# Performance work log

Measured on AMD Instinct MI355X. Metric: run time of the kernel, lower is better.

## Reference

```python
import jax, jax.numpy as jnp
import numpy as np

N_HEADS = 32
N_KV_HEADS = 8
HEAD_DIM = 128
HIDDEN = 4096
ROPE_BASE = 10000.0


def _rope_tables(seq_len, head_dim, base):
    inv_freq = 1.0 / (base ** (jnp.arange(0, head_dim, 2, dtype=jnp.float32) / head_dim))
    t = jnp.arange(seq_len, dtype=jnp.float32)
    freqs = jnp.outer(t, inv_freq)                    # (S, D/2)
    emb = jnp.concatenate([freqs, freqs], axis=-1)    # (S, D)
    return jnp.cos(emb), jnp.sin(emb)


def _rotate_half(x):
    half = x.shape[-1] // 2
    return jnp.concatenate([-x[..., half:], x[..., :half]], axis=-1)


def _apply_rope(x, cos, sin):
    # x: (B, H, S, D); cos/sin: (S, D)
    return x * cos[None, None] + _rotate_half(x) * sin[None, None]


def setup_inputs() -> dict:
    key = jax.random.key(0)
    k1, k2, k3 = jax.random.split(key, 3)
    bsz, q_len = 2, 2048
    total_heads = N_HEADS + 2 * N_KV_HEADS
    hidden_states = jax.random.normal(k1, (bsz, q_len, HIDDEN), dtype=jnp.float32)
    w_qkv = jax.random.normal(k2, (total_heads * HEAD_DIM, HIDDEN), dtype=jnp.float32) * 0.02
    w_o = jax.random.normal(k3, (HIDDEN, N_HEADS * HEAD_DIM), dtype=jnp.float32) * 0.02
    return {"hidden_states": hidden_states, "w_qkv": w_qkv, "w_o": w_o}


def reference(hidden_states, w_qkv, w_o):
    bsz, q_len, _ = hidden_states.shape
    n_rep = N_HEADS // N_KV_HEADS

    qkv = jnp.einsum('bsh,oh->bso', hidden_states, w_qkv)  # (B, S, total_heads*D)
    q_sz = N_HEADS * HEAD_DIM
    kv_sz = N_KV_HEADS * HEAD_DIM
    q = qkv[..., :q_sz].reshape(bsz, q_len, N_HEADS, HEAD_DIM).transpose(0, 2, 1, 3)
    k = qkv[..., q_sz:q_sz + kv_sz].reshape(bsz, q_len, N_KV_HEADS, HEAD_DIM).transpose(0, 2, 1, 3)
    v = qkv[..., q_sz + kv_sz:].reshape(bsz, q_len, N_KV_HEADS, HEAD_DIM).transpose(0, 2, 1, 3)

    cos, sin = _rope_tables(q_len, HEAD_DIM, ROPE_BASE)
    q = _apply_rope(q, cos, sin)
    k = _apply_rope(k, cos, sin)

    # repeat KV heads for GQA
    k = jnp.repeat(k, n_rep, axis=1)  # (B, H, S, D)
    v = jnp.repeat(v, n_rep, axis=1)

    scale = HEAD_DIM ** -0.5
    scores = jnp.einsum('bhqd,bhkd->bhqk', q, k) * scale
    causal = jnp.tril(jnp.ones((q_len, q_len), dtype=bool))
    scores = jnp.where(causal[None, None], scores, jnp.finfo(scores.dtype).min)
    attn = jax.nn.softmax(scores, axis=-1)
    out = jnp.einsum('bhqk,bhkd->bhqd', attn, v)  # (B, H, S, D)
    out = out.transpose(0, 2, 1, 3).reshape(bsz, q_len, N_HEADS * HEAD_DIM)
    return jnp.einsum('bso,ho->bsh', out, w_o)
```

## Files before the change

kernel.cpp:

```cpp
#include <hip/hip_runtime.h>
#include <stdint.h>

#define N_HEADS   32
#define N_KV      8
#define HEAD_DIM  128
#define HIDDEN_DIM 4096
#define BSZ       2
#define SEQ       2048
#define TOT_HEADS 48
#define QKV_DIM   6144
#define ROWS      4096
#define ROPE_HEADS 40

typedef __attribute__((ext_vector_type(4)))  float f32x4;
typedef __attribute__((ext_vector_type(16))) float f32x16;
typedef __attribute__((ext_vector_type(8)))  short bf16x8;
typedef unsigned short u16;
typedef unsigned int   u32;

#define AS1 __attribute__((address_space(1)))
#define AS3 __attribute__((address_space(3)))

static __device__ __forceinline__ float bf16f(u16 u) { return __uint_as_float(((u32)u) << 16); }
static __device__ __forceinline__ u16 f2bf(float f) {
  u32 x = __float_as_uint(f);
  x += 0x7fffu + ((x >> 16) & 1u);
  return (u16)(x >> 16);
}
static __device__ __forceinline__ u32 cvt_pk_bf16(float lo, float hi) {
  u32 r;
  asm("v_cvt_pk_bf16_f32 %0, %1, %2" : "=v"(r) : "v"(lo), "v"(hi));
  return r;
}
static __device__ __forceinline__ bf16x8 mk8(u32 a, u32 b, u32 c, u32 d) {
  union { u32 u[4]; bf16x8 v; } x;
  x.u[0] = a; x.u[1] = b; x.u[2] = c; x.u[3] = d;
  return x.v;
}
static __device__ __forceinline__ void pl32swap(u32& a, u32& b) {
  asm("v_permlane32_swap_b32 %0, %1" : "+v"(a), "+v"(b));
}
static __device__ __forceinline__ float crosshalf_max(float v) {
  u32 xa = __float_as_uint(v), xb;
  asm("v_mov_b32 %0, %1" : "=v"(xb) : "v"(xa));
  pl32swap(xa, xb);
  return fmaxf(__uint_as_float(xa), __uint_as_float(xb));
}
static __device__ __forceinline__ float crosshalf_sum(float v) {
  u32 xa = __float_as_uint(v), xb;
  asm("v_mov_b32 %0, %1" : "=v"(xb) : "v"(xa));
  pl32swap(xa, xb);
  return __uint_as_float(xa) + __uint_as_float(xb);
}

#define SB0()   __builtin_amdgcn_sched_barrier(0)
#define SBAR()  do { __builtin_amdgcn_sched_barrier(0); __builtin_amdgcn_s_barrier(); \
                     __builtin_amdgcn_sched_barrier(0); } while (0)
#define LGKM(n) do { asm volatile("s_waitcnt lgkmcnt(" #n ")" ::: "memory"); \
                     __builtin_amdgcn_sched_barrier(0); } while (0)

__global__ void cast3_k(const float4* __restrict__ a, const float4* __restrict__ b,
                        const float4* __restrict__ c,
                        ushort4* __restrict__ oa, ushort4* __restrict__ ob,
                        ushort4* __restrict__ oc, int na, int nb, int nc) {
  int i = blockIdx.x * blockDim.x + threadIdx.x;
  const int stride = gridDim.x * blockDim.x;
  const int tot = na + nb + nc;
  for (; i < tot; i += stride) {
    const float4* s; ushort4* d; int j = i;
    if (j < na)           { s = a; d = oa; }
    else if (j < na + nb) { s = b; d = ob; j -= na; }
    else                  { s = c; d = oc; j -= na + nb; }
    const float4 v = s[j];
    ushort4 o;
    o.x = f2bf(v.x); o.y = f2bf(v.y); o.z = f2bf(v.z); o.w = f2bf(v.w);
    d[j] = o;
  }
}

__global__ void rope_tables_k(float* __restrict__ ctab, float* __restrict__ stab) {
  int t = blockIdx.x * blockDim.x + threadIdx.x;
  if (t >= SEQ * 64) return;
  int s = t >> 6, i = t & 63;
  float inv = powf(10000.0f, -(float)i / 64.0f);
  float ang = (float)s * inv;
  float sv, cv;
  sincosf(ang, &sv, &cv);
  ctab[t] = cv; stab[t] = sv;
}

template<int F32OUT>
__global__ __launch_bounds__(256, 2)
void gemm_bt_k(const u16* __restrict__ A, const u16* __restrict__ Bw,
               void* __restrict__ C, int M, int N, int K, int ldc)
{
  __shared__ uint4 smA[1024];
  __shared__ uint4 smB[1024];
  const int tid = threadIdx.x;
  const int nbx = N >> 7;
  const int bm = (blockIdx.x / nbx) << 7;
  const int bn = (blockIdx.x % nbx) << 7;
  const int lane = tid & 63;
  const int wave = tid >> 6;
  const int wm = (wave >> 1) << 6;
  const int wn = (wave & 1) << 6;
  const int fr = lane & 15;
  const int fq = lane >> 4;

  f32x4 acc[4][4];
#pragma unroll
  for (int i = 0; i < 4; ++i)
#pragma unroll
    for (int j = 0; j < 4; ++j)
      acc[i][j] = {0.f, 0.f, 0.f, 0.f};

  const int gl_r = lane >> 3;
  const int gl_c = (lane & 7) ^ gl_r;

  for (int k0 = 0; k0 < K; k0 += 64) {
#pragma unroll
    for (int i = 0; i < 4; ++i) {
      const int rbase = (wave << 5) + (i << 3);
      const int row = rbase + gl_r;
      const u16* gA = A  + (size_t)(bm + row) * K + k0 + (gl_c << 3);
      const u16* gB = Bw + (size_t)(bn + row) * K + k0 + (gl_c << 3);
      __builtin_amdgcn_global_load_lds((const AS1 u32*)gA, (AS3 u32*)&smA[rbase << 3], 16, 0, 0);
      __builtin_amdgcn_global_load_lds((const AS1 u32*)gB, (AS3 u32*)&smB[rbase << 3], 16, 0, 0);
    }
    __syncthreads();
#pragma unroll
    for (int kk = 0; kk < 2; ++kk) {
      bf16x8 af[4], bfr[4];
      const int cc = (kk << 2) + fq;
#pragma unroll
      for (int m = 0; m < 4; ++m) {
        const int row = wm + (m << 4) + fr;
        af[m] = *reinterpret_cast<const bf16x8*>(&smA[(row << 3) + (cc ^ (row & 7))]);
      }
#pragma unroll
      for (int n = 0; n < 4; ++n) {
        const int row = wn + (n << 4) + fr;
        bfr[n] = *reinterpret_cast<const bf16x8*>(&smB[(row << 3) + (cc ^ (row & 7))]);
      }
#pragma unroll
      for (int m = 0; m < 4; ++m)
#pragma unroll
        for (int n = 0; n < 4; ++n)
          acc[m][n] = __builtin_amdgcn_mfma_f32_16x16x32_bf16(af[m], bfr[n], acc[m][n], 0, 0, 0);
    }
    __syncthreads();
  }

  const int col0 = bn + wn + fr;
#pragma unroll
  for (int m = 0; m < 4; ++m) {
#pragma unroll
    for (int i = 0; i < 4; ++i) {
      const int row = bm + wm + (m << 4) + (fq << 2) + i;
      if (F32OUT) {
        float* rp = reinterpret_cast<float*>(C) + (size_t)row * ldc + col0;
#pragma unroll
        for (int n = 0; n < 4; ++n) rp[n << 4] = acc[m][n][i];
      } else {
        u16* rp = reinterpret_cast<u16*>(C) + (size_t)row * ldc + col0;
#pragma unroll
        for (int n = 0; n < 4; ++n) rp[n << 4] = f2bf(acc[m][n][i]);
      }
    }
  }
}

template<int F32OUT>
__global__ __launch_bounds__(512, 2)
void gemm256_k(const u16* __restrict__ A, const u16* __restrict__ Bw,
               void* __restrict__ C, int M, int N, int K, int ldc)
{
  extern __shared__ uint4 lds[];
  uint4* LA = lds;
  uint4* LB = lds + 4096;
  const int NT = K >> 6;
  const int tid  = threadIdx.x;
  const int lane = tid & 63;
  const int wave = tid >> 6;
  const int nbx = N >> 8;
  const int cpx = gridDim.x >> 3;
  const int wg  = (blockIdx.x & 7) * cpx + (blockIdx.x >> 3);
  const int bm = (wg / nbx) << 8;
  const int bn = (wg % nbx) << 8;

  const int wm = (wave >> 2) << 7;
  const int wn = (wave & 3) << 6;
  const int fr = lane & 15;
  const int fq = lane >> 4;
  const int s7 = fr & 7;

  const int rA  = (wave << 3) + (lane >> 3);
  const int c8e = (((lane & 7) ^ (lane >> 3)) << 3);

  auto SA = [&](int t, int h, int buf) {
    uint4* d = LA + (buf << 11) + (h << 10) + (wave << 6);
    const u16* s = A + (size_t)(bm + (h << 7) + rA) * K + (t << 6) + c8e;
    __builtin_amdgcn_global_load_lds((const AS1 u32*)s, (AS3 u32*)d, 16, 0, 0);
    __builtin_amdgcn_global_load_lds((const AS1 u32*)(s + (size_t)64 * K), (AS3 u32*)(d + 512), 16, 0, 0);
  };
  auto SB = [&](int t, int h, int buf) {
    uint4* d = LB + (buf << 11) + (h << 10) + (wave << 6);
    const u16* s = Bw + (size_t)(bn + (h << 7) + rA) * K + (t << 6) + c8e;
    __builtin_amdgcn_global_load_lds((const AS1 u32*)s, (AS3 u32*)d, 16, 0, 0);
    __builtin_amdgcn_global_load_lds((const AS1 u32*)(s + (size_t)64 * K), (AS3 u32*)(d + 512), 16, 0, 0);
  };

  f32x4 acc[8][4];
#pragma unroll
  for (int m = 0; m < 8; ++m)
#pragma unroll
    for (int n = 0; n < 4; ++n)
      acc[m][n] = {0.f, 0.f, 0.f, 0.f};

  SB(0, 0, 0); SB(0, 1, 0); SA(0, 0, 0); SA(0, 1, 0);
  SB(1, 0, 1); SB(1, 1, 1); SA(1, 0, 1);
  asm volatile("s_waitcnt vmcnt(6)" ::: "memory");
  SBAR();

  bf16x8 Af0[4][2], Af1[4][2], B0[2][2], B1[2][2];

#pragma unroll 1
  for (int t = 0; t < NT; ++t) {
    const int buf  = t & 1;
    const int base = buf << 11;
    const int abase = base + ((wm + fr) << 3);
    const int bbase = base + ((wn + fr) << 3);

#pragma unroll
    for (int m = 0; m < 4; ++m)
#pragma unroll
      for (int kk = 0; kk < 2; ++kk)
        Af0[m][kk] = *reinterpret_cast<const bf16x8*>(&LA[abase + m * 128 + (((kk << 2) + fq) ^ s7)]);
#pragma unroll
    for (int n = 0; n < 2; ++n)
#pragma unroll
      for (int kk = 0; kk < 2; ++kk)
        B0[n][kk] = *reinterpret_cast<const bf16x8*>(&LB[bbase + n * 128 + (((kk << 2) + fq) ^ s7)]);
    SB0();
#pragma unroll
    for (int n = 0; n < 2; ++n)
#pragma unroll
      for (int kk = 0; kk < 2; ++kk)
        B1[n][kk] = *reinterpret_cast<const bf16x8*>(&LB[bbase + (2 + n) * 128 + (((kk << 2) + fq) ^ s7)]);
    SB0();
#pragma unroll
    for (int m = 0; m < 4; ++m)
#pragma unroll
      for (int kk = 0; kk < 2; ++kk)
        Af1[m][kk] = *reinterpret_cast<const bf16x8*>(&LA[abase + 512 + m * 128 + (((kk << 2) + fq) ^ s7)]);
    SB0();

    if (t + 1 < NT) SA(t + 1, 1, buf ^ 1);
    SBAR();

    LGKM(12);
    __builtin_amdgcn_s_setprio(1);
#pragma unroll
    for (int m = 0; m < 4; ++m)
#pragma unroll
      for (int n = 0; n < 2; ++n)
#pragma unroll
        for (int kk = 0; kk < 2; ++kk)
          acc[m][n] = __builtin_amdgcn_mfma_f32_16x16x32_bf16(Af0[m][kk], B0[n][kk], acc[m][n], 0, 0, 0);
    __builtin_amdgcn_s_setprio(0);
    SBAR();

    LGKM(8);
    __builtin_amdgcn_s_setprio(1);
#pragma unroll
    for (int m = 0; m < 4; ++m)
#pragma unroll
      for (int n = 0; n < 2; ++n)
#pragma unroll
        for (int kk = 0; kk < 2; ++kk)
          acc[m][2 + n] = __builtin_amdgcn_mfma_f32_16x16x32_bf16(Af0[m][kk], B1[n][kk], acc[m][2 + n], 0, 0, 0);
    __builtin_amdgcn_s_setprio(0);
    if (t + 2 < NT) SB(t + 2, 0, buf);
    SBAR();

    LGKM(0);
    __builtin_amdgcn_s_setprio(1);
#pragma unroll
    for (int m = 0; m < 4; ++m)
#pragma unroll
      for (int n = 0; n < 2; ++n)
#pragma unroll
        for (int kk = 0; kk < 2; ++kk)
          acc[4 + m][2 + n] = __builtin_amdgcn_mfma_f32_16x16x32_bf16(Af1[m][kk], B1[n][kk], acc[4 + m][2 + n], 0, 0, 0);
    __builtin_amdgcn_s_setprio(0);
    SBAR();

    if (t + 2 < NT) { SB(t + 2, 1, buf); SA(t + 2, 0, buf); }
    __builtin_amdgcn_s_setprio(1);
#pragma unroll
    for (int m = 0; m < 4; ++m)
#pragma unroll
      for (int n = 0; n < 2; ++n)
#pragma unroll
        for (int kk = 0; kk < 2; ++kk)
          acc[4 + m][n] = __builtin_amdgcn_mfma_f32_16x16x32_bf16(Af1[m][kk], B0[n][kk], acc[4 + m][n], 0, 0, 0);
    __builtin_amdgcn_s_setprio(0);
    if (t < NT - 2)       { asm volatile("s_waitcnt vmcnt(6)" ::: "memory"); }
    else if (t == NT - 2) { asm volatile("s_waitcnt vmcnt(0)" ::: "memory"); }
    SBAR();
  }

  const int col0 = bn + wn + fr;
#pragma unroll
  for (int m = 0; m < 8; ++m) {
#pragma unroll
    for (int i = 0; i < 4; ++i) {
      const int row = bm + wm + (m << 4) + (fq << 2) + i;
      if (F32OUT) {
        float* rp = reinterpret_cast<float*>(C) + (size_t)row * ldc + col0;
#pragma unroll
        for (int n = 0; n < 4; ++n) rp[n << 4] = acc[m][n][i];
      } else {
        u16* rp = reinterpret_cast<u16*>(C) + (size_t)row * ldc + col0;
#pragma unroll
        for (int n = 0; n < 4; ++n) rp[n << 4] = f2bf(acc[m][n][i]);
      }
    }
  }
}

__global__ void rope_scatter_k(const u16* __restrict__ QKV,
                               const float* __restrict__ ctab, const float* __restrict__ stab,
                               u16* __restrict__ Qo, u16* __restrict__ Ko)
{
  const int t = blockIdx.x * blockDim.x + threadIdx.x;
  const int d = t & 63;
  const int hh = (t >> 6) % ROPE_HEADS;
  const int row = t / (64 * ROPE_HEADS);
  const int b = row >> 11, sq = row & (SEQ - 1);
  const u16* src = QKV + (size_t)row * QKV_DIM + hh * HEAD_DIM;
  const float x1 = bf16f(src[d]);
  const float x2 = bf16f(src[d + 64]);
  const float c = ctab[(sq << 6) + d], sn = stab[(sq << 6) + d];
  float y1 = x1 * c - x2 * sn;
  float y2 = x2 * c + x1 * sn;
  u16* dst;
  if (hh < N_HEADS) {
    const float SC2 = 0.1275170747f;
    y1 *= SC2; y2 *= SC2;
    dst = Qo + ((size_t)(b * N_HEADS + hh) * SEQ + sq) * HEAD_DIM;
  } else {
    dst = Ko + ((size_t)(b * N_KV + (hh - N_HEADS)) * SEQ + sq) * HEAD_DIM;
  }
  dst[d] = f2bf(y1);
  dst[d + 64] = f2bf(y2);
}

__global__ __launch_bounds__(256)
void vtrans_k(const u16* __restrict__ QKV, u16* __restrict__ Vt)
{
  __shared__ u16 tile[64][72];
  const int idx = blockIdx.x;
  const int dt = idx & 1;
  const int st = (idx >> 1) & 31;
  const int kv = (idx >> 6) & 7;
  const int b  = idx >> 9;
  const int tid = threadIdx.x;
  const int s0 = st << 6, d0 = dt << 6;
  const int rl = tid >> 3, cc8 = (tid & 7) << 3;
#pragma unroll
  for (int p = 0; p < 2; ++p) {
    const int sl = rl + (p << 5);
    const u16* src = QKV + (size_t)(b * SEQ + s0 + sl) * QKV_DIM
                   + (N_HEADS + N_KV + kv) * HEAD_DIM + d0 + cc8;
    *reinterpret_cast<uint4*>(&tile[sl][cc8]) = *reinterpret_cast<const uint4*>(src);
  }
  __syncthreads();
#pragma unroll
  for (int p = 0; p < 2; ++p) {
    const int dl = rl + (p << 5);
    u16 tmp[8];
#pragma unroll
    for (int k2 = 0; k2 < 8; ++k2) tmp[k2] = tile[cc8 + k2][dl];
    u16* dst = Vt + ((size_t)(b * N_KV + kv) * HEAD_DIM + d0 + dl) * SEQ + s0 + cc8;
    *reinterpret_cast<uint4*>(dst) = *reinterpret_cast<const uint4*>(tmp);
  }
}

__global__ __launch_bounds__(512, 2)
void attn_mfma_k(const u16* __restrict__ Q, const u16* __restrict__ K,
                 const u16* __restrict__ Vt, u16* __restrict__ Out)
{
  __shared__ uint4 Ksm[2][512];
  __shared__ uint4 Vsm[2][512];
  const int tid  = threadIdx.x;
  const int lane = tid & 63;
  const int w    = tid >> 6;
  const int idx  = blockIdx.x;
  const int kvh  = idx & 7;
  const int b    = (idx >> 3) & 1;
  const int qi   = 31 - (idx >> 4);
  const int q0   = qi << 6;
  const int head = w & 3;
  const int qsub = w >> 2;
  const int h    = (kvh << 2) + head;
  const int diag = 2 * qi + qsub;
  const int nsub = 2 * qi + 2;

  const int ql = lane & 31;
  const int hh = lane >> 5;

  const u16* Qh = Q  + (size_t)(b * N_HEADS + h) * SEQ * HEAD_DIM;
  const u16* Kb = K  + (size_t)(b * N_KV + kvh) * SEQ * HEAD_DIM;
  const u16* Vb = Vt + (size_t)(b * N_KV + kvh) * HEAD_DIM * SEQ;

  int koff[8];
#pragma unroll
  for (int f = 0; f < 8; ++f) koff[f] = (ql << 4) + (((f << 1) + hh) ^ (ql & 15));
  int voff0[4], voff1[4];
#pragma unroll
  for (int dblk = 0; dblk < 4; ++dblk) {
    const int d = (dblk << 5) + ql;
    voff0[dblk] = (d << 2) + ((hh + (d >> 1)) & 3);
    voff1[dblk] = (d << 2) + ((2 + hh + (d >> 1)) & 3);
  }

  auto stage = [&](int buf, int ks) {
    const int sl = (w << 6) + lane;
    {
      const int row = sl >> 4, cs = sl & 15;
      const int g = cs ^ (row & 15);
      const u16* src = Kb + (size_t)(ks + row) * HEAD_DIM + (g << 3);
      __builtin_amdgcn_global_load_lds((const AS1 u32*)src, (AS3 u32*)&Ksm[buf][w << 6], 16, 0, 0);
    }
    {
      const int d = sl >> 2, cs = sl & 3;
      const int g = (cs - (d >> 1)) & 3;
      const u16* src = Vb + (size_t)d * SEQ + ks + (g << 3);
      __builtin_amdgcn_global_load_lds((const AS1 u32*)src, (AS3 u32*)&Vsm[buf][w << 6], 16, 0, 0);
    }
  };

  bf16x8 qf[8];
#pragma unroll
  for (int f = 0; f < 8; ++f)
    qf[f] = *reinterpret_cast<const bf16x8*>(Qh + (size_t)(q0 + (qsub << 5) + ql) * HEAD_DIM
                                             + 16 * f + 8 * hh);

  f32x16 o[4];
#pragma unroll
  for (int dblk = 0; dblk < 4; ++dblk)
#pragma unroll
    for (int r = 0; r < 16; ++r) o[dblk][r] = 0.f;
  float m2 = -1e30f, lsum = 0.f;

  stage(0, 0);

#pragma unroll 1
  for (int s = 0; s < nsub; ++s) {
    const int cur = s & 1;
    __syncthreads();
    if (s + 1 < nsub) stage(cur ^ 1, (s + 1) << 5);

    if (s <= diag) {
      f32x16 T;
#pragma unroll
      for (int r = 0; r < 16; ++r) T[r] = 0.f;
      __builtin_amdgcn_s_setprio(1);
#pragma unroll
      for (int f = 0; f < 8; ++f) {
        const bf16x8 kf = *reinterpret_cast<const bf16x8*>(&Ksm[cur][koff[f]]);
        T = __builtin_amdgcn_mfma_f32_32x32x16_bf16(kf, qf[f], T, 0, 0, 0);
      }
      __builtin_amdgcn_s_setprio(0);

      if (s == diag) {
#pragma unroll
        for (int r = 0; r < 16; ++r) {
          const int kr = (r & 3) + ((r >> 2) << 3) + (hh << 2);
          if (kr > ql) T[r] = -1e30f;
        }
      }
      float mx[8];
#pragma unroll
      for (int r = 0; r < 8; ++r) mx[r] = fmaxf(T[2 * r], T[2 * r + 1]);
#pragma unroll
      for (int r = 0; r < 4; ++r) mx[r] = fmaxf(mx[r], mx[r + 4]);
      mx[0] = fmaxf(mx[0], mx[2]);
      mx[1] = fmaxf(mx[1], mx[3]);
      const float mt = crosshalf_max(fmaxf(mx[0], mx[1]));

      if (__any(mt > m2 + 8.f)) {
        const float mnew = fmaxf(m2, mt);
        const float resc = exp2f(m2 - mnew);
        lsum *= resc;
#pragma unroll
        for (int r = 0; r < 16; ++r) {
          const int qr = (r & 3) + ((r >> 2) << 3) + (hh << 2);
          const float rr = __shfl(resc, qr);
#pragma unroll
          for (int dblk = 0; dblk < 4; ++dblk) o[dblk][r] *= rr;
        }
        m2 = mnew;
      }

      float ps = 0.f;
#pragma unroll
      for (int r = 0; r < 16; ++r) { const float pv = exp2f(T[r] - m2); T[r] = pv; ps += pv; }
      lsum += crosshalf_sum(ps);

      u32 pk[8];
#pragma unroll
      for (int i = 0; i < 8; ++i)
        pk[i] = cvt_pk_bf16(T[2 * i], T[2 * i + 1]);
      pl32swap(pk[0], pk[2]); pl32swap(pk[1], pk[3]);
      pl32swap(pk[4], pk[6]); pl32swap(pk[5], pk[7]);
      const bf16x8 a0 = mk8(pk[0], pk[1], pk[2], pk[3]);
      const bf16x8 a1 = mk8(pk[4], pk[5], pk[6], pk[7]);

      __builtin_amdgcn_s_setprio(1);
#pragma unroll
      for (int dblk = 0; dblk < 4; ++dblk) {
        const bf16x8 va = *reinterpret_cast<const bf16x8*>(&Vsm[cur][voff0[dblk]]);
        o[dblk] = __builtin_amdgcn_mfma_f32_32x32x16_bf16(a0, va, o[dblk], 0, 0, 0);
        const bf16x8 vb2 = *reinterpret_cast<const bf16x8*>(&Vsm[cur][voff1[dblk]]);
        o[dblk] = __builtin_amdgcn_mfma_f32_32x32x16_bf16(a1, vb2, o[dblk], 0, 0, 0);
      }
      __builtin_amdgcn_s_setprio(0);
    }
  }

  u16* Ob = Out + (size_t)(b * SEQ + q0 + (qsub << 5)) * HIDDEN_DIM + h * HEAD_DIM + ql;
#pragma unroll
  for (int r = 0; r < 16; ++r) {
    const int qr = (r & 3) + ((r >> 2) << 3) + (hh << 2);
    const float il = 1.0f / __shfl(lsum, qr);
    u16* rp = Ob + (size_t)qr * HIDDEN_DIM;
#pragma unroll
    for (int dblk = 0; dblk < 4; ++dblk)
      rp[dblk * 32] = f2bf(o[dblk][r] * il);
  }
}

extern "C" void kernel_launch(void* const* d_in, const int* in_sizes, int n_in,
                              void* d_out, int out_size, void* d_ws, size_t ws_size,
                              hipStream_t stream)
{
  const float* hs   = (const float*)d_in[0];
  const float* wqkv = (const float*)d_in[1];
  const float* wo   = (const float*)d_in[2];
  float* out = (float*)d_out;
  char* ws = (char*)d_ws;
  size_t off = 0;
  auto alloc = [&](size_t bytes) -> void* {
    void* p = ws + off;
    off += (bytes + 255) & ~(size_t)255;
    return p;
  };
  u16* Xbf    = (u16*)alloc((size_t)ROWS * HIDDEN_DIM * 2);
  u16* Wqkvbf = (u16*)alloc((size_t)QKV_DIM * HIDDEN_DIM * 2);
  u16* Wobf   = (u16*)alloc((size_t)HIDDEN_DIM * HIDDEN_DIM * 2);
  u16* QKVbf  = (u16*)alloc((size_t)ROWS * QKV_DIM * 2);
  u16* Qbf    = (u16*)alloc((size_t)BSZ * N_HEADS * SEQ * HEAD_DIM * 2);
  u16* Kbf    = (u16*)alloc((size_t)BSZ * N_KV * SEQ * HEAD_DIM * 2);
  u16* Vtbf   = (u16*)alloc((size_t)BSZ * N_KV * SEQ * HEAD_DIM * 2);
  float* ctab = (float*)alloc((size_t)SEQ * 64 * 4);
  float* stab = (float*)alloc((size_t)SEQ * 64 * 4);
  u16* AOut   = (u16*)alloc((size_t)ROWS * HIDDEN_DIM * 2);
  if (off > ws_size) return;

  (void)hipFuncSetAttribute(reinterpret_cast<const void*>(&gemm256_k<0>),
                            hipFuncAttributeMaxDynamicSharedMemorySize, 131072);
  (void)hipFuncSetAttribute(reinterpret_cast<const void*>(&gemm256_k<1>),
                            hipFuncAttributeMaxDynamicSharedMemorySize, 131072);

  cast3_k<<<4096, 256, 0, stream>>>((const float4*)hs, (const float4*)wqkv, (const float4*)wo,
                                    (ushort4*)Xbf, (ushort4*)Wqkvbf, (ushort4*)Wobf,
                                    ROWS * HIDDEN_DIM / 4, QKV_DIM * HIDDEN_DIM / 4,
                                    HIDDEN_DIM * HIDDEN_DIM / 4);
  rope_tables_k<<<(SEQ * 64) / 256, 256, 0, stream>>>(ctab, stab);

  gemm256_k<0><<<(ROWS / 256) * (4096 / 256), 512, 131072, stream>>>(
      Xbf, Wqkvbf, (void*)QKVbf, ROWS, 4096, HIDDEN_DIM, QKV_DIM);
  gemm_bt_k<0><<<(ROWS / 128) * (2048 / 128), 256, 0, stream>>>(
      Xbf, Wqkvbf + (size_t)4096 * HIDDEN_DIM, (void*)(QKVbf + 4096),
      ROWS, 2048, HIDDEN_DIM, QKV_DIM);

  rope_scatter_k<<<ROWS * ROPE_HEADS * 64 / 256, 256, 0, stream>>>(QKVbf, ctab, stab, Qbf, Kbf);
  vtrans_k<<<BSZ * N_KV * (SEQ / 64) * (HEAD_DIM / 64), 256, 0, stream>>>(QKVbf, Vtbf);
  attn_mfma_k<<<BSZ * N_KV * (SEQ / 64), 512, 0, stream>>>(Qbf, Kbf, Vtbf, AOut);
  gemm256_k<1><<<(ROWS / 256) * (HIDDEN_DIM / 256), 512, 131072, stream>>>(
      AOut, Wobf, (void*)out, ROWS, HIDDEN_DIM, HIDDEN_DIM, HIDDEN_DIM);
}
```

Baseline: 521.1 us.

## Widen attention KV tile to 64 keys per stage with two score blocks

```diff
diff --git a/kernel.cpp b/kernel.cpp
--- a/kernel.cpp
+++ b/kernel.cpp
@@ -387,12 +387,12 @@
   }
 }
 
-__global__ __launch_bounds__(512, 2)
+__global__ __launch_bounds__(512, 4)
 void attn_mfma_k(const u16* __restrict__ Q, const u16* __restrict__ K,
                  const u16* __restrict__ Vt, u16* __restrict__ Out)
 {
-  __shared__ uint4 Ksm[2][512];
-  __shared__ uint4 Vsm[2][512];
+  __shared__ uint4 Ksm[2][1024];
+  __shared__ uint4 Vsm[2][1024];
   const int tid  = threadIdx.x;
   const int lane = tid & 63;
   const int w    = tid >> 6;
@@ -404,8 +404,6 @@
   const int head = w & 3;
   const int qsub = w >> 2;
   const int h    = (kvh << 2) + head;
-  const int diag = 2 * qi + qsub;
-  const int nsub = 2 * qi + 2;
 
   const int ql = lane & 31;
   const int hh = lane >> 5;
@@ -417,27 +415,31 @@
   int koff[8];
 #pragma unroll
   for (int f = 0; f < 8; ++f) koff[f] = (ql << 4) + (((f << 1) + hh) ^ (ql & 15));
-  int voff0[4], voff1[4];
-#pragma unroll
-  for (int dblk = 0; dblk < 4; ++dblk) {
-    const int d = (dblk << 5) + ql;
-    voff0[dblk] = (d << 2) + ((hh + (d >> 1)) & 3);
-    voff1[dblk] = (d << 2) + ((2 + hh + (d >> 1)) & 3);
-  }
+  int voff[4][4];
+#pragma unroll
+  for (int dblk = 0; dblk < 4; ++dblk)
+#pragma unroll
+    for (int j = 0; j < 4; ++j)
+      voff[dblk][j] = ((((dblk << 5) + ql) << 3)) + (((j << 1) + hh + ql) & 7);
 
   auto stage = [&](int buf, int ks) {
-    const int sl = (w << 6) + lane;
-    {
-      const int row = sl >> 4, cs = sl & 15;
+#pragma unroll
+    for (int p = 0; p < 2; ++p) {
+      const int base = (p << 9) + (w << 6);
+      const int sl2 = base + lane;
+      const int row = sl2 >> 4, cs = sl2 & 15;
       const int g = cs ^ (row & 15);
       const u16* src = Kb + (size_t)(ks + row) * HEAD_DIM + (g << 3);
-      __builtin_amdgcn_global_load_lds((const AS1 u32*)src, (AS3 u32*)&Ksm[buf][w << 6], 16, 0, 0);
-    }
-    {
-      const int d = sl >> 2, cs = sl & 3;
-      const int g = (cs - (d >> 1)) & 3;
+      __builtin_amdgcn_global_load_lds((const AS1 u32*)src, (AS3 u32*)&Ksm[buf][base], 16, 0, 0);
+    }
+#pragma unroll
+    for (int p = 0; p < 2; ++p) {
+      const int base = (p << 9) + (w << 6);
+      const int sl2 = base + lane;
+      const int d = sl2 >> 3, cs = sl2 & 7;
+      const int g = (cs - d) & 7;
       const u16* src = Vb + (size_t)d * SEQ + ks + (g << 3);
-      __builtin_amdgcn_global_load_lds((const AS1 u32*)src, (AS3 u32*)&Vsm[buf][w << 6], 16, 0, 0);
+      __builtin_amdgcn_global_load_lds((const AS1 u32*)src, (AS3 u32*)&Vsm[buf][base], 16, 0, 0);
     }
   };
 
@@ -457,77 +459,93 @@
   stage(0, 0);
 
 #pragma unroll 1
-  for (int s = 0; s < nsub; ++s) {
-    const int cur = s & 1;
+  for (int sb = 0; sb <= qi; ++sb) {
+    const int cur = sb & 1;
     __syncthreads();
-    if (s + 1 < nsub) stage(cur ^ 1, (s + 1) << 5);
-
-    if (s <= diag) {
-      f32x16 T;
-#pragma unroll
-      for (int r = 0; r < 16; ++r) T[r] = 0.f;
-      __builtin_amdgcn_s_setprio(1);
-#pragma unroll
-      for (int f = 0; f < 8; ++f) {
-        const bf16x8 kf = *reinterpret_cast<const bf16x8*>(&Ksm[cur][koff[f]]);
-        T = __builtin_amdgcn_mfma_f32_32x32x16_bf16(kf, qf[f], T, 0, 0, 0);
+    if (sb < qi) stage(cur ^ 1, (sb + 1) << 6);
+
+    f32x16 T0, T1;
+#pragma unroll
+    for (int r = 0; r < 16; ++r) { T0[r] = 0.f; T1[r] = 0.f; }
+    __builtin_amdgcn_s_setprio(1);
+#pragma unroll
+    for (int f = 0; f < 8; ++f) {
+      const bf16x8 kf = *reinterpret_cast<const bf16x8*>(&Ksm[cur][koff[f]]);
+      T0 = __builtin_amdgcn_mfma_f32_32x32x16_bf16(kf, qf[f], T0, 0, 0, 0);
+    }
+#pragma unroll
+    for (int f = 0; f < 8; ++f) {
+      const bf16x8 kf = *reinterpret_cast<const bf16x8*>(&Ksm[cur][koff[f] + 512]);
+      T1 = __builtin_amdgcn_mfma_f32_32x32x16_bf16(kf, qf[f], T1, 0, 0, 0);
+    }
+    __builtin_amdgcn_s_setprio(0);
+
+    if (sb == qi) {
+      const int limit = (qsub << 5) + ql;
+#pragma unroll
+      for (int r = 0; r < 16; ++r) {
+        const int kr = (r & 3) + ((r >> 2) << 3) + (hh << 2);
+        if (kr > limit)      T0[r] = -1e30f;
+        if (kr + 32 > limit) T1[r] = -1e30f;
       }
-      __builtin_amdgcn_s_setprio(0);
-
-      if (s == diag) {
-#pragma unroll
-        for (int r = 0; r < 16; ++r) {
-          const int kr = (r & 3) + ((r >> 2) << 3) + (hh << 2);
-          if (kr > ql) T[r] = -1e30f;
-        }
+    }
+    float mx[8];
+#pragma unroll
+    for (int r = 0; r < 8; ++r)
+      mx[r] = fmaxf(fmaxf(T0[2 * r], T0[2 * r + 1]), fmaxf(T1[2 * r], T1[2 * r + 1]));
+#pragma unroll
+    for (int r = 0; r < 4; ++r) mx[r] = fmaxf(mx[r], mx[r + 4]);
+    mx[0] = fmaxf(mx[0], mx[2]);
+    mx[1] = fmaxf(mx[1], mx[3]);
+    const float mt = crosshalf_max(fmaxf(mx[0], mx[1]));
+
+    if (__any(mt > m2 + 8.f)) {
+      const float mnew = fmaxf(m2, mt);
+      const float resc = exp2f(m2 - mnew);
+      lsum *= resc;
+#pragma unroll
+      for (int r = 0; r < 16; ++r) {
+        const int qr = (r & 3) + ((r >> 2) << 3) + (hh << 2);
+        const float rr = __shfl(resc, qr);
+#pragma unroll
+        for (int dblk = 0; dblk < 4; ++dblk) o[dblk][r] *= rr;
       }
-      float mx[8];
-#pragma unroll
-      for (int r = 0; r < 8; ++r) mx[r] = fmaxf(T[2 * r], T[2 * r + 1]);
-#pragma unroll
-      for (int r = 0; r < 4; ++r) mx[r] = fmaxf(mx[r], mx[r + 4]);
-      mx[0] = fmaxf(mx[0], mx[2]);
-      mx[1] = fmaxf(mx[1], mx[3]);
-      const float mt = crosshalf_max(fmaxf(mx[0], mx[1]));
-
-      if (__any(mt > m2 + 8.f)) {
-        const float mnew = fmaxf(m2, mt);
-        const float resc = exp2f(m2 - mnew);
-        lsum *= resc;
-#pragma unroll
-        for (int r = 0; r < 16; ++r) {
-          const int qr = (r & 3) + ((r >> 2) << 3) + (hh << 2);
-          const float rr = __shfl(resc, qr);
-#pragma unroll
-          for (int dblk = 0; dblk < 4; ++dblk) o[dblk][r] *= rr;
-        }
-        m2 = mnew;
+      m2 = mnew;
+    }
+
+    float ps = 0.f;
+#pragma unroll
+    for (int r = 0; r < 16; ++r) {
+      const float p0 = exp2f(T0[r] - m2); T0[r] = p0; ps += p0;
+      const float p1 = exp2f(T1[r] - m2); T1[r] = p1; ps += p1;
+    }
+    lsum += crosshalf_sum(ps);
+
+    u32 pk[16];
+#pragma unroll
+    for (int i = 0; i < 8; ++i) {
+      pk[i]     = cvt_pk_bf16(T0[2 * i], T0[2 * i + 1]);
+      pk[8 + i] = cvt_pk_bf16(T1[2 * i], T1[2 * i + 1]);
+    }
+    pl32swap(pk[0], pk[2]);  pl32swap(pk[1], pk[3]);
+    pl32swap(pk[4], pk[6]);  pl32swap(pk[5], pk[7]);
+    pl32swap(pk[8], pk[10]); pl32swap(pk[9], pk[11]);
+    pl32swap(pk[12], pk[14]); pl32swap(pk[13], pk[15]);
+    bf16x8 a[4];
+    a[0] = mk8(pk[0], pk[1], pk[2], pk[3]);
+    a[1] = mk8(pk[4], pk[5], pk[6], pk[7]);
+    a[2] = mk8(pk[8], pk[9], pk[10], pk[11]);
+    a[3] = mk8(pk[12], pk[13], pk[14], pk[15]);
+
+    __builtin_amdgcn_s_setprio(1);
+#pragma unroll
+    for (int dblk = 0; dblk < 4; ++dblk)
+#pragma unroll
+      for (int j = 0; j < 4; ++j) {
+        const bf16x8 vb = *reinterpret_cast<const bf16x8*>(&Vsm[cur][voff[dblk][j]]);
+        o[dblk] = __builtin_amdgcn_mfma_f32_32x32x16_bf16(a[j], vb, o[dblk], 0, 0, 0);
       }
-
-      float ps = 0.f;
-#pragma unroll
-      for (int r = 0; r < 16; ++r) { const float pv = exp2f(T[r] - m2); T[r] = pv; ps += pv; }
-      lsum += crosshalf_sum(ps);
-
-      u32 pk[8];
-#pragma unroll
-      for (int i = 0; i < 8; ++i)
-        pk[i] = cvt_pk_bf16(T[2 * i], T[2 * i + 1]);
-      pl32swap(pk[0], pk[2]); pl32swap(pk[1], pk[3]);
-      pl32swap(pk[4], pk[6]); pl32swap(pk[5], pk[7]);
-      const bf16x8 a0 = mk8(pk[0], pk[1], pk[2], pk[3]);
-      const bf16x8 a1 = mk8(pk[4], pk[5], pk[6], pk[7]);
-
-      __builtin_amdgcn_s_setprio(1);
-#pragma unroll
-      for (int dblk = 0; dblk < 4; ++dblk) {
-        const bf16x8 va = *reinterpret_cast<const bf16x8*>(&Vsm[cur][voff0[dblk]]);
-        o[dblk] = __builtin_amdgcn_mfma_f32_32x32x16_bf16(a0, va, o[dblk], 0, 0, 0);
-        const bf16x8 vb2 = *reinterpret_cast<const bf16x8*>(&Vsm[cur][voff1[dblk]]);
-        o[dblk] = __builtin_amdgcn_mfma_f32_32x32x16_bf16(a1, vb2, o[dblk], 0, 0, 0);
-      }
-      __builtin_amdgcn_s_setprio(0);
-    }
+    __builtin_amdgcn_s_setprio(0);
   }
 
   u16* Ob = Out + (size_t)(b * SEQ + q0 + (qsub << 5)) * HIDDEN_DIM + h * HEAD_DIM + ql;
```

After: 777.8 us. 49.3% more time.
